# Performance work log

Measured on AMD Instinct MI355X. Metric: run time of the kernel, lower is better.

The kernel has to match this reference:

```python
import jax, jax.numpy as jnp
import numpy as np

B, S, E, H, D, W = 2, 4096, 512, 8, 64, 512
NUM_BUCKETS, MAX_DISTANCE = 32, 128  # hardcoded in get_relative_positions for 't5'
NEG_INF = -1e30


def _t5_bucket_causal(relative_position):
    """T5 relative position bucketing, unidirectional (causal)."""
    n = jnp.maximum(-relative_position, 0)
    max_exact = NUM_BUCKETS // 2
    is_small = n < max_exact
    nf = jnp.maximum(n.astype(jnp.float32), 1.0)
    val_if_large = max_exact + (
        jnp.log(nf / max_exact) / np.log(MAX_DISTANCE / max_exact)
        * (NUM_BUCKETS - max_exact)
    ).astype(jnp.int32)
    val_if_large = jnp.minimum(val_if_large, NUM_BUCKETS - 1)
    return jnp.where(is_small, n, val_if_large)


def setup_inputs() -> dict:
    key = jax.random.key(0)
    ks = jax.random.split(key, 7)
    scale = 1.0 / np.sqrt(E)  # keep logits in a sane range
    return {
        'xs': jax.random.normal(ks[0], (B, S, E), jnp.float32),
        'prev_k': jax.random.normal(ks[1], (B, W, H, D), jnp.float32),
        'prev_v': jax.random.normal(ks[2], (B, W, H, D), jnp.float32),
        'w_q': jax.random.normal(ks[3], (E, H, D), jnp.float32) * scale,
        'w_k': jax.random.normal(ks[4], (E, H, D), jnp.float32) * scale,
        'w_v': jax.random.normal(ks[5], (E, H, D), jnp.float32) * scale,
        'rel_bias': jax.random.normal(ks[6], (H, NUM_BUCKETS), jnp.float32),
    }


def reference(xs, prev_k, prev_v, w_q, w_k, w_v, rel_bias):
    nw = S // W  # number of windows
    # kvq projections; queries pre-scaled by 1/sqrt(head_size)
    q = jnp.einsum('bse,ehd->bshd', xs, w_q) * (1.0 / np.sqrt(D))
    k = jnp.einsum('bse,ehd->bshd', xs, w_k)
    v = jnp.einsum('bse,ehd->bshd', xs, w_v)
    qw = q.reshape(B, nw, W, H, D)
    kw = k.reshape(B, nw, W, H, D)
    vw = v.reshape(B, nw, W, H, D)
    # Transformer-XL sliding window: keys for window i = [window i-1 keys ; window i keys]
    k_prev = jnp.concatenate([prev_k[:, None], kw[:, :-1]], axis=1)  # (B,nw,W,H,D)
    v_prev = jnp.concatenate([prev_v[:, None], vw[:, :-1]], axis=1)
    k2 = jnp.concatenate([k_prev, kw], axis=2)  # (B,nw,2W,H,D)
    v2 = jnp.concatenate([v_prev, vw], axis=2)
    # T5 relative position bias and causal mask (num_queries=W, num_keys=2W)
    ctx = jnp.arange(W)[:, None] + W          # query absolute position in key frame
    mem = jnp.arange(2 * W)[None, :]
    relpos = mem - ctx                        # (W, 2W), key - query
    bias = rel_bias[:, _t5_bucket_causal(relpos)]  # (H, W, 2W)
    # causal + window mask: key j attends iff i < j <= i+W (each query sees exactly W keys)
    mask = (relpos <= 0) & (relpos > -W)
    # attention per window
    scores = jnp.einsum('bnqhd,bnkhd->bnhqk', qw, k2)  # (B,nw,H,W,2W)
    scores = scores + bias[None, None]
    scores = jnp.where(mask[None, None, None], scores, NEG_INF)
    probs = jax.nn.softmax(scores, axis=-1)
    attn = jnp.einsum('bnhqk,bnkhd->bnqhd', probs, v2)
    attn_ys = attn.reshape(B, S, H, D)
    # next_kvi cache = last window's keys/values
    next_k = kw[:, -1]
    next_v = vw[:, -1]
    return attn_ys, next_k, next_v
```

## Files before the change

### kernel.cpp

```cpp
#include <hip/hip_runtime.h>
#include <hip/hip_bf16.h>
#include <math.h>

#define B_ 2
#define S_ 4096
#define E_ 512
#define H_ 8
#define D_ 64
#define W_ 512
#define NW_ 8

#define MASKV -1e30f
#define MINIT -1e4f

typedef float f32x4 __attribute__((ext_vector_type(4)));
typedef short s16x4 __attribute__((ext_vector_type(4)));
typedef short s16x8 __attribute__((ext_vector_type(8)));
typedef unsigned int u32;
typedef __attribute__((address_space(1))) const u32 as1_u32;
typedef __attribute__((address_space(3))) u32 as3_u32;

__device__ inline short f2bf(float f) {
    unsigned u = __builtin_bit_cast(unsigned, f);
    unsigned r = (u + 0x7FFFu + ((u >> 16) & 1u)) >> 16;
    return (short)r;
}
__device__ inline s16x8 pack8(f32x4 a, f32x4 b) {
    s16x8 r;
    r[0]=f2bf(a[0]); r[1]=f2bf(a[1]); r[2]=f2bf(a[2]); r[3]=f2bf(a[3]);
    r[4]=f2bf(b[0]); r[5]=f2bf(b[1]); r[6]=f2bf(b[2]); r[7]=f2bf(b[3]);
    return r;
}
__device__ __forceinline__ void gl_lds16(const void* g, void* l) {
    __builtin_amdgcn_global_load_lds((as1_u32*)(unsigned long long)g,
                                     (as3_u32*)(u32)(unsigned long long)l,
                                     16, 0, 0);
}

__global__ void convert_kernel(const float* __restrict__ xs, const float* __restrict__ pk,
                               const float* __restrict__ pv, short* __restrict__ xsbf,
                               short* __restrict__ pkbf, short* __restrict__ pvbf)
{
    size_t i8 = ((size_t)blockIdx.x * 256 + threadIdx.x) * 8;
    const float* src; short* dst; size_t off;
    if (i8 < 4194304)            { src = xs; dst = xsbf; off = i8; }
    else if (i8 < 4194304+524288){ src = pk; dst = pkbf; off = i8 - 4194304; }
    else                         { src = pv; dst = pvbf; off = i8 - 4194304 - 524288; }
    f32x4 a = *(const f32x4*)(src + off);
    f32x4 b = *(const f32x4*)(src + off + 4);
    *(s16x8*)(dst + off) = pack8(a, b);
}

__global__ void transpose_w_kernel(const float* __restrict__ wq, const float* __restrict__ wk,
                                   const float* __restrict__ wv, short* __restrict__ wt)
{
    __shared__ float st[64][68];
    const int k0 = blockIdx.x * 64;
    const int nt = blockIdx.y;
    const int z  = nt >> 3;
    const int n0 = (nt & 7) * 64;
    const float* wz = (z == 0) ? wq : (z == 1) ? wk : wv;
    const float scale = (z == 0) ? 0.125f : 1.0f;
    const int tid = threadIdx.x;
    {
        int kk = tid >> 4, nn = (tid & 15) * 4;
        #pragma unroll
        for (int it = 0; it < 4; ++it) {
            f32x4 x = *(const f32x4*)(wz + (size_t)(k0 + kk + it * 16) * 512 + n0 + nn);
            *(f32x4*)&st[kk + it * 16][nn] = x;
        }
    }
    __syncthreads();
    {
        int nn2 = tid >> 2, kseg = (tid & 3) * 16;
        s16x8 o0, o1;
        #pragma unroll
        for (int j = 0; j < 8; ++j) o0[j] = f2bf(st[kseg + j][nn2] * scale);
        #pragma unroll
        for (int j = 0; j < 8; ++j) o1[j] = f2bf(st[kseg + 8 + j][nn2] * scale);
        short* dst = wt + (size_t)(z * 512 + n0 + nn2) * 512 + k0 + kseg;
        *(s16x8*)(dst) = o0;
        *(s16x8*)(dst + 8) = o1;
    }
}

__global__ __launch_bounds__(256, 4)
void proj_kernel(const short* __restrict__ xsbf, const short* __restrict__ wt,
                 short* __restrict__ qkvbf, float* __restrict__ out)
{
    __shared__ short Xs[128][64];
    __shared__ short Ws[128][64];

    const int tid = threadIdx.x;
    const int m0  = blockIdx.x * 128;
    const int n0  = blockIdx.y * 128;
    const int z   = n0 >> 9;
    const int ln0 = n0 & 511;
    const int wave = tid >> 6, lane = tid & 63;
    const int wq = (wave & 1) * 64;
    const int wx = (wave >> 1) * 64;
    const int lr = lane & 15, quad = lane >> 4;

    f32x4 acc[4][4] = {};

    const int r8  = lane >> 3;
    const int gr  = lane & 7;

    for (int k0 = 0; k0 < 512; k0 += 64) {
        #pragma unroll
        for (int i = 0; i < 4; ++i) {
            int row = 32 * wave + 8 * i + r8;
            int gs  = gr ^ (row & 7);
            gl_lds16(xsbf + (size_t)(m0 + row) * 512 + k0 + gs * 8, &Xs[32 * wave + 8 * i][0]);
            gl_lds16(wt   + (size_t)(n0 + row) * 512 + k0 + gs * 8, &Ws[32 * wave + 8 * i][0]);
        }
        __syncthreads();
        #pragma unroll
        for (int ks = 0; ks < 2; ++ks) {
            s16x8 af[4], bf[4];
            #pragma unroll
            for (int ta = 0; ta < 4; ++ta) {
                int R = wq + ta * 16 + lr;
                af[ta] = *(const s16x8*)&Ws[R][(((ks * 4 + quad) ^ (R & 7)) * 8)];
            }
            #pragma unroll
            for (int tb = 0; tb < 4; ++tb) {
                int R = wx + tb * 16 + lr;
                bf[tb] = *(const s16x8*)&Xs[R][(((ks * 4 + quad) ^ (R & 7)) * 8)];
            }
            #pragma unroll
            for (int ta = 0; ta < 4; ++ta)
                #pragma unroll
                for (int tb = 0; tb < 4; ++tb)
                    acc[ta][tb] = __builtin_amdgcn_mfma_f32_16x16x32_bf16(
                        af[ta], bf[tb], acc[ta][tb], 0, 0, 0);
        }
        __syncthreads();
    }

    short* base = qkvbf + (size_t)z * ((size_t)8192 * 512);
    #pragma unroll
    for (int ta = 0; ta < 4; ++ta)
        #pragma unroll
        for (int tb = 0; tb < 4; ++tb) {
            int m  = m0 + wx + tb * 16 + lr;
            int ln = ln0 + wq + ta * 16 + quad * 4;
            s16x4 o;
            o[0] = f2bf(acc[ta][tb][0]); o[1] = f2bf(acc[ta][tb][1]);
            o[2] = f2bf(acc[ta][tb][2]); o[3] = f2bf(acc[ta][tb][3]);
            *(s16x4*)(base + (size_t)m * 512 + ln) = o;
            if (z != 0 && (m & 4095) >= 3584) {
                int bb = m >> 12, rr = (m & 4095) - 3584;
                float* dst = out + 4194304 + (size_t)(z - 1) * 524288
                           + ((size_t)(bb * 512 + rr)) * 512 + ln;
                *(f32x4*)dst = acc[ta][tb];
            }
        }
}

__global__ __launch_bounds__(512, 4)
void attn_kernel(const short* __restrict__ qkvbf, const short* __restrict__ pkbf,
                 const short* __restrict__ pvbf, const float* __restrict__ rel_bias,
                 float* __restrict__ out)
{
    __shared__ short p_s[128][72];
    __shared__ short k_s[2][64][72];
    __shared__ short vt_s[2][64][72];
    __shared__ float bias_s[512];

    const short* qb = qkvbf;
    const short* kb = qkvbf + (size_t)8192 * 512;
    const short* vb = qkvbf + (size_t)2 * 8192 * 512;

    const int bid = blockIdx.x;
    const int qt = bid & 3;
    const int h  = (bid >> 2) & 7;
    const int n  = (bid >> 5) & 7;
    const int b  = bid >> 8;
    const int tid = threadIdx.x;
    const int wave = tid >> 6, lane = tid & 63;
    const int lr = lane & 15, quad = lane >> 4;
    const int q0 = qt * 128;
    const int i0 = q0 + 16 * wave;

    {
        int nd = tid;
        int bucket;
        if (nd < 16) bucket = nd;
        else {
            int vbk = 16 + (int)(log((double)nd * (1.0 / 16.0)) * (16.0 / log(8.0)));
            bucket = vbk < 31 ? vbk : 31;
        }
        bias_s[nd] = rel_bias[h * 32 + bucket];
    }

    s16x8 aq[2];
    {
        const short* src = qb + (size_t)(b * S_ + n * W_ + i0 + lr) * 512 + h * 64 + quad * 8;
        aq[0] = *(const s16x8*)(src);
        aq[1] = *(const s16x8*)(src + 32);
    }

    f32x4 oacc[4] = {};
    float m_r[4], l_r[4];
    #pragma unroll
    for (int rg = 0; rg < 4; ++rg) { m_r[rg] = MINIT; l_r[rg] = 0.f; }

    const int cmin = (16 * wave) >> 6;
    int cmax = (16 * wave + 528) >> 6; if (cmax > 9) cmax = 9;

    const int ksr = tid >> 3;
    const int ksd = (tid & 7) * 8;
    const int vkey = tid & 63;
    const int vd0 = (tid >> 6) * 8;

    s16x8 rk, rv;
    {
        int jj = q0 + ksr;
        int p  = n * W_ + jj - W_;
        const short* ks = (p >= 0) ? kb + (size_t)(b * S_ + p) * 512 + h * 64 + ksd
                                   : pkbf + ((size_t)(b * W_ + jj) * H_ + h) * D_ + ksd;
        rk = *(const s16x8*)ks;
        int jv = q0 + vkey;
        int pv = n * W_ + jv - W_;
        const short* vs = (pv >= 0) ? vb + (size_t)(b * S_ + pv) * 512 + h * 64 + vd0
                                    : pvbf + ((size_t)(b * W_ + jv) * H_ + h) * D_ + vd0;
        rv = *(const s16x8*)vs;
    }

    for (int c = 0; c < 10; ++c) {
        const int pb = c & 1;
        *(s16x8*)&k_s[pb][ksr][ksd] = rk;
        #pragma unroll
        for (int m = 0; m < 8; ++m) vt_s[pb][vd0 + m][vkey] = rv[m];

        {
            int cn = (c < 9) ? c + 1 : 9;
            int jj = q0 + 64 * cn + ksr;
            int p  = n * W_ + jj - W_;
            const short* ks = (p >= 0) ? kb + (size_t)(b * S_ + p) * 512 + h * 64 + ksd
                                       : pkbf + ((size_t)(b * W_ + jj) * H_ + h) * D_ + ksd;
            rk = *(const s16x8*)ks;
            int jv = q0 + 64 * cn + vkey;
            int pv = n * W_ + jv - W_;
            const short* vs = (pv >= 0) ? vb + (size_t)(b * S_ + pv) * 512 + h * 64 + vd0
                                        : pvbf + ((size_t)(b * W_ + jv) * H_ + h) * D_ + vd0;
            rv = *(const s16x8*)vs;
        }

        __syncthreads();
        if (c < cmin || c > cmax) continue;

        f32x4 sacc[4] = {};
        #pragma unroll
        for (int ks = 0; ks < 2; ++ks) {
            s16x8 bk[4];
            #pragma unroll
            for (int tn = 0; tn < 4; ++tn)
                bk[tn] = *(const s16x8*)&k_s[pb][tn * 16 + lr][ks * 32 + quad * 8];
            #pragma unroll
            for (int tn = 0; tn < 4; ++tn)
                sacc[tn] = __builtin_amdgcn_mfma_f32_16x16x32_bf16(
                    aq[ks], bk[tn], sacc[tn], 0, 0, 0);
        }

        const int jc = q0 + 64 * c + lr;
        #pragma unroll
        for (int tn = 0; tn < 4; ++tn) {
            int j = jc + tn * 16;
            #pragma unroll
            for (int rg = 0; rg < 4; ++rg) {
                int i = i0 + quad * 4 + rg;
                unsigned dm1 = (unsigned)(j - i - 1);
                int nd = (i + 512 - j) & 511;
                float sv = sacc[tn][rg] + bias_s[nd];
                sacc[tn][rg] = (dm1 < 512u) ? sv : MASKV;
            }
        }

        float rmax[4];
        #pragma unroll
        for (int rg = 0; rg < 4; ++rg)
            rmax[rg] = fmaxf(fmaxf(sacc[0][rg], sacc[1][rg]),
                             fmaxf(sacc[2][rg], sacc[3][rg]));
        #pragma unroll
        for (int off = 1; off < 16; off <<= 1)
            #pragma unroll
            for (int rg = 0; rg < 4; ++rg)
                rmax[rg] = fmaxf(rmax[rg], __shfl_xor(rmax[rg], off));

        float al[4], rs[4];
        #pragma unroll
        for (int rg = 0; rg < 4; ++rg) {
            float mo = m_r[rg];
            float mn = fmaxf(mo, rmax[rg]);
            al[rg] = __expf(mo - mn);
            m_r[rg] = mn;
            rs[rg] = 0.f;
        }

        #pragma unroll
        for (int tn = 0; tn < 4; ++tn)
            #pragma unroll
            for (int rg = 0; rg < 4; ++rg) {
                float p = __expf(sacc[tn][rg] - m_r[rg]);
                rs[rg] += p;
                p_s[16 * wave + quad * 4 + rg][tn * 16 + lr] = f2bf(p);
            }

        #pragma unroll
        for (int off = 1; off < 16; off <<= 1)
            #pragma unroll
            for (int rg = 0; rg < 4; ++rg)
                rs[rg] += __shfl_xor(rs[rg], off);

        #pragma unroll
        for (int rg = 0; rg < 4; ++rg)
            l_r[rg] = l_r[rg] * al[rg] + rs[rg];

        #pragma unroll
        for (int tn = 0; tn < 4; ++tn)
            #pragma unroll
            for (int rg = 0; rg < 4; ++rg)
                oacc[tn][rg] *= al[rg];

        asm volatile("s_waitcnt lgkmcnt(0)" ::: "memory");

        #pragma unroll
        for (int ks = 0; ks < 2; ++ks) {
            s16x8 ap = *(const s16x8*)&p_s[16 * wave + lr][ks * 32 + quad * 8];
            s16x8 bv[4];
            #pragma unroll
            for (int tn = 0; tn < 4; ++tn)
                bv[tn] = *(const s16x8*)&vt_s[pb][tn * 16 + lr][ks * 32 + quad * 8];
            #pragma unroll
            for (int tn = 0; tn < 4; ++tn)
                oacc[tn] = __builtin_amdgcn_mfma_f32_16x16x32_bf16(
                    ap, bv[tn], oacc[tn], 0, 0, 0);
        }
    }

    #pragma unroll
    for (int rg = 0; rg < 4; ++rg) {
        int row = i0 + quad * 4 + rg;
        float linv = 1.0f / l_r[rg];
        float* dst = out + (((size_t)b * S_ + n * W_ + row) * H_ + h) * D_ + lr;
        #pragma unroll
        for (int tn = 0; tn < 4; ++tn)
            dst[tn * 16] = oacc[tn][rg] * linv;
    }
}

extern "C" void kernel_launch(void* const* d_in, const int* in_sizes, int n_in,
                              void* d_out, int out_size, void* d_ws, size_t ws_size,
                              hipStream_t stream)
{
    const float* xs       = (const float*)d_in[0];
    const float* prev_k   = (const float*)d_in[1];
    const float* prev_v   = (const float*)d_in[2];
    const float* w_q      = (const float*)d_in[3];
    const float* w_k      = (const float*)d_in[4];
    const float* w_v      = (const float*)d_in[5];
    const float* rel_bias = (const float*)d_in[6];
    float* out = (float*)d_out;

    short* xsbf  = (short*)d_ws;
    short* wt    = xsbf + (size_t)8192 * 512;
    short* qkvbf = wt + (size_t)1536 * 512;
    short* pkbf  = qkvbf + (size_t)3 * 8192 * 512;
    short* pvbf  = pkbf + (size_t)524288;

    convert_kernel<<<2560, 256, 0, stream>>>(xs, prev_k, prev_v, xsbf, pkbf, pvbf);
    transpose_w_kernel<<<dim3(8, 24), 256, 0, stream>>>(w_q, w_k, w_v, wt);

    proj_kernel<<<dim3(64, 12), 256, 0, stream>>>(xsbf, wt, qkvbf, out);

    attn_kernel<<<512, 512, 0, stream>>>(qkvbf, pkbf, pvbf, rel_bias, out);
}
```

Measured before the change: 146.8 us.

## Store V transposed, async-load K/V to swizzled LDS, drop online softmax max

The projection kernel now writes V in a head-dim-major transposed layout, and a new small kernel converts and transposes prev_v into the same layout. The attention kernel fetches K and V^T straight into XOR-swizzled LDS with global_load_lds double buffering, replacing the register staging and scalar LDS transpose. The online softmax no longer tracks a running max: it exponentiates the biased scores directly and, for far chunks, uses the constant bucket-31 bias instead of a table lookup. Skipping the max relies on the logits staying small and risks overflow for other inputs.

```diff
diff --git a/kernel.cpp b/kernel.cpp
--- a/kernel.cpp
+++ b/kernel.cpp
@@ -4,14 +4,11 @@
 
 #define B_ 2
 #define S_ 4096
-#define E_ 512
 #define H_ 8
 #define D_ 64
 #define W_ 512
-#define NW_ 8
 
 #define MASKV -1e30f
-#define MINIT -1e4f
 
 typedef float f32x4 __attribute__((ext_vector_type(4)));
 typedef short s16x4 __attribute__((ext_vector_type(4)));
@@ -36,19 +33,49 @@
                                      (as3_u32*)(u32)(unsigned long long)l,
                                      16, 0, 0);
 }
+__device__ __forceinline__ void drain_vmem() {
+    asm volatile("s_waitcnt vmcnt(0)" ::: "memory");
+}
 
 __global__ void convert_kernel(const float* __restrict__ xs, const float* __restrict__ pk,
-                               const float* __restrict__ pv, short* __restrict__ xsbf,
-                               short* __restrict__ pkbf, short* __restrict__ pvbf)
+                               short* __restrict__ xsbf, short* __restrict__ pkbf)
 {
     size_t i8 = ((size_t)blockIdx.x * 256 + threadIdx.x) * 8;
     const float* src; short* dst; size_t off;
-    if (i8 < 4194304)            { src = xs; dst = xsbf; off = i8; }
-    else if (i8 < 4194304+524288){ src = pk; dst = pkbf; off = i8 - 4194304; }
-    else                         { src = pv; dst = pvbf; off = i8 - 4194304 - 524288; }
+    if (i8 < 4194304) { src = xs; dst = xsbf; off = i8; }
+    else              { src = pk; dst = pkbf; off = i8 - 4194304; }
     f32x4 a = *(const f32x4*)(src + off);
     f32x4 b = *(const f32x4*)(src + off + 4);
     *(s16x8*)(dst + off) = pack8(a, b);
+}
+
+__global__ void prev_v_t_kernel(const float* __restrict__ pv, short* __restrict__ vbt)
+{
+    __shared__ short st[64][72];
+    const int bidx = blockIdx.x;
+    const int jt = bidx & 7, h = (bidx >> 3) & 7, b = bidx >> 6;
+    const int jj0 = jt * 64;
+    const int tid = threadIdx.x;
+    {
+        int kk = tid >> 2, d0 = (tid & 3) * 16;
+        const float* src = pv + (((size_t)(b * 512 + jj0 + kk)) * 8 + h) * 64 + d0;
+        f32x4 x0 = *(const f32x4*)(src);
+        f32x4 x1 = *(const f32x4*)(src + 4);
+        f32x4 x2 = *(const f32x4*)(src + 8);
+        f32x4 x3 = *(const f32x4*)(src + 12);
+        *(s16x8*)&st[kk][d0]     = pack8(x0, x1);
+        *(s16x8*)&st[kk][d0 + 8] = pack8(x2, x3);
+    }
+    __syncthreads();
+    {
+        int dd = tid >> 2, k0 = (tid & 3) * 16;
+        s16x8 o0, o1;
+        #pragma unroll
+        for (int t = 0; t < 8; ++t) { o0[t] = st[k0 + t][dd]; o1[t] = st[k0 + 8 + t][dd]; }
+        short* dst = vbt + (size_t)(h * 64 + dd) * 9216 + b * 4608 + jj0 + k0;
+        *(s16x8*)dst = o0;
+        *(s16x8*)(dst + 8) = o1;
+    }
 }
 
 __global__ void transpose_w_kernel(const float* __restrict__ wq, const float* __restrict__ wk,
@@ -86,7 +113,8 @@
 
 __global__ __launch_bounds__(256, 4)
 void proj_kernel(const short* __restrict__ xsbf, const short* __restrict__ wt,
-                 short* __restrict__ qkvbf, float* __restrict__ out)
+                 short* __restrict__ qkbf, short* __restrict__ vbt,
+                 float* __restrict__ out)
 {
     __shared__ short Xs[128][64];
     __shared__ short Ws[128][64];
@@ -114,6 +142,7 @@
             gl_lds16(xsbf + (size_t)(m0 + row) * 512 + k0 + gs * 8, &Xs[32 * wave + 8 * i][0]);
             gl_lds16(wt   + (size_t)(n0 + row) * 512 + k0 + gs * 8, &Ws[32 * wave + 8 * i][0]);
         }
+        drain_vmem();
         __syncthreads();
         #pragma unroll
         for (int ks = 0; ks < 2; ++ks) {
@@ -138,39 +167,48 @@
         __syncthreads();
     }
 
-    short* base = qkvbf + (size_t)z * ((size_t)8192 * 512);
     #pragma unroll
     for (int ta = 0; ta < 4; ++ta)
         #pragma unroll
         for (int tb = 0; tb < 4; ++tb) {
             int m  = m0 + wx + tb * 16 + lr;
             int ln = ln0 + wq + ta * 16 + quad * 4;
-            s16x4 o;
-            o[0] = f2bf(acc[ta][tb][0]); o[1] = f2bf(acc[ta][tb][1]);
-            o[2] = f2bf(acc[ta][tb][2]); o[3] = f2bf(acc[ta][tb][3]);
-            *(s16x4*)(base + (size_t)m * 512 + ln) = o;
-            if (z != 0 && (m & 4095) >= 3584) {
-                int bb = m >> 12, rr = (m & 4095) - 3584;
-                float* dst = out + 4194304 + (size_t)(z - 1) * 524288
-                           + ((size_t)(bb * 512 + rr)) * 512 + ln;
-                *(f32x4*)dst = acc[ta][tb];
+            int bb = m >> 12, seq = m & 4095;
+            if (z < 2) {
+                short* base = qkbf + (size_t)z * ((size_t)8192 * 512);
+                s16x4 o;
+                o[0] = f2bf(acc[ta][tb][0]); o[1] = f2bf(acc[ta][tb][1]);
+                o[2] = f2bf(acc[ta][tb][2]); o[3] = f2bf(acc[ta][tb][3]);
+                *(s16x4*)(base + (size_t)m * 512 + ln) = o;
+                if (z == 1 && seq >= 3584) {
+                    float* dst = out + 4194304 + ((size_t)(bb * 512 + seq - 3584)) * 512 + ln;
+                    *(f32x4*)dst = acc[ta][tb];
+                }
+            } else {
+                size_t col = (size_t)bb * 4608 + 512 + seq;
+                #pragma unroll
+                for (int g = 0; g < 4; ++g)
+                    vbt[(size_t)(ln + g) * 9216 + col] = f2bf(acc[ta][tb][g]);
+                if (seq >= 3584) {
+                    float* dst = out + 4194304 + 524288 + ((size_t)(bb * 512 + seq - 3584)) * 512 + ln;
+                    *(f32x4*)dst = acc[ta][tb];
+                }
             }
         }
 }
 
 __global__ __launch_bounds__(512, 4)
-void attn_kernel(const short* __restrict__ qkvbf, const short* __restrict__ pkbf,
-                 const short* __restrict__ pvbf, const float* __restrict__ rel_bias,
+void attn_kernel(const short* __restrict__ qkbf, const short* __restrict__ vbt,
+                 const short* __restrict__ pkbf, const float* __restrict__ rel_bias,
                  float* __restrict__ out)
 {
-    __shared__ short p_s[128][72];
-    __shared__ short k_s[2][64][72];
-    __shared__ short vt_s[2][64][72];
+    __shared__ short k_s[2][64][64];
+    __shared__ short vt_s[2][64][64];
+    __shared__ short p_s[128][64];
     __shared__ float bias_s[512];
 
-    const short* qb = qkvbf;
-    const short* kb = qkvbf + (size_t)8192 * 512;
-    const short* vb = qkvbf + (size_t)2 * 8192 * 512;
+    const short* qb = qkbf;
+    const short* kb = qkbf + (size_t)8192 * 512;
 
     const int bid = blockIdx.x;
     const int qt = bid & 3;
@@ -193,6 +231,7 @@
         }
         bias_s[nd] = rel_bias[h * 32 + bucket];
     }
+    const float bias31 = rel_bias[h * 32 + 31];
 
     s16x8 aq[2];
     {
@@ -202,53 +241,34 @@
     }
 
     f32x4 oacc[4] = {};
-    float m_r[4], l_r[4];
-    #pragma unroll
-    for (int rg = 0; rg < 4; ++rg) { m_r[rg] = MINIT; l_r[rg] = 0.f; }
+    float lsum = 0.f;
 
     const int cmin = (16 * wave) >> 6;
-    int cmax = (16 * wave + 528) >> 6; if (cmax > 9) cmax = 9;
-
-    const int ksr = tid >> 3;
-    const int ksd = (tid & 7) * 8;
-    const int vkey = tid & 63;
-    const int vd0 = (tid >> 6) * 8;
-
-    s16x8 rk, rv;
-    {
-        int jj = q0 + ksr;
+    const int cmax = (16 * wave + 527) >> 6;
+
+    const int r8 = lane >> 3, gr = lane & 7;
+
+    auto issueKV = [&](int c, int pb) {
+        int jj = q0 + 64 * c + 8 * wave + r8;
         int p  = n * W_ + jj - W_;
-        const short* ks = (p >= 0) ? kb + (size_t)(b * S_ + p) * 512 + h * 64 + ksd
-                                   : pkbf + ((size_t)(b * W_ + jj) * H_ + h) * D_ + ksd;
-        rk = *(const s16x8*)ks;
-        int jv = q0 + vkey;
-        int pv = n * W_ + jv - W_;
-        const short* vs = (pv >= 0) ? vb + (size_t)(b * S_ + pv) * 512 + h * 64 + vd0
-                                    : pvbf + ((size_t)(b * W_ + jv) * H_ + h) * D_ + vd0;
-        rv = *(const s16x8*)vs;
-    }
+        int gs = gr ^ r8;
+        const short* ksrc = (p >= 0)
+            ? kb   + ((size_t)(b * S_ + p)) * 512 + h * 64 + gs * 8
+            : pkbf + (((size_t)(b * W_ + jj)) * 8 + h) * 64 + gs * 8;
+        gl_lds16(ksrc, &k_s[pb][8 * wave][0]);
+        int drow = 8 * wave + r8;
+        const short* vsrc = vbt + (size_t)(h * 64 + drow) * 9216
+                          + b * 4608 + n * W_ + q0 + 64 * c + gs * 8;
+        gl_lds16(vsrc, &vt_s[pb][8 * wave][0]);
+    };
+
+    issueKV(0, 0);
 
     for (int c = 0; c < 10; ++c) {
         const int pb = c & 1;
-        *(s16x8*)&k_s[pb][ksr][ksd] = rk;
-        #pragma unroll
-        for (int m = 0; m < 8; ++m) vt_s[pb][vd0 + m][vkey] = rv[m];
-
-        {
-            int cn = (c < 9) ? c + 1 : 9;
-            int jj = q0 + 64 * cn + ksr;
-            int p  = n * W_ + jj - W_;
-            const short* ks = (p >= 0) ? kb + (size_t)(b * S_ + p) * 512 + h * 64 + ksd
-                                       : pkbf + ((size_t)(b * W_ + jj) * H_ + h) * D_ + ksd;
-            rk = *(const s16x8*)ks;
-            int jv = q0 + 64 * cn + vkey;
-            int pv = n * W_ + jv - W_;
-            const short* vs = (pv >= 0) ? vb + (size_t)(b * S_ + pv) * 512 + h * 64 + vd0
-                                        : pvbf + ((size_t)(b * W_ + jv) * H_ + h) * D_ + vd0;
-            rv = *(const s16x8*)vs;
-        }
-
+        drain_vmem();
         __syncthreads();
+        if (c < 9) issueKV(c + 1, pb ^ 1);
         if (c < cmin || c > cmax) continue;
 
         f32x4 sacc[4] = {};
@@ -257,82 +277,60 @@
             s16x8 bk[4];
             #pragma unroll
             for (int tn = 0; tn < 4; ++tn)
-                bk[tn] = *(const s16x8*)&k_s[pb][tn * 16 + lr][ks * 32 + quad * 8];
+                bk[tn] = *(const s16x8*)&k_s[pb][tn * 16 + lr][(((4 * ks + quad) ^ (lr & 7)) * 8)];
             #pragma unroll
             for (int tn = 0; tn < 4; ++tn)
                 sacc[tn] = __builtin_amdgcn_mfma_f32_16x16x32_bf16(
-                    aq[ks], bk[tn], sacc[tn], 0, 0, 0);
-        }
-
-        const int jc = q0 + 64 * c + lr;
-        #pragma unroll
-        for (int tn = 0; tn < 4; ++tn) {
-            int j = jc + tn * 16;
-            #pragma unroll
-            for (int rg = 0; rg < 4; ++rg) {
-                int i = i0 + quad * 4 + rg;
-                unsigned dm1 = (unsigned)(j - i - 1);
-                int nd = (i + 512 - j) & 511;
-                float sv = sacc[tn][rg] + bias_s[nd];
-                sacc[tn][rg] = (dm1 < 512u) ? sv : MASKV;
-            }
-        }
-
-        float rmax[4];
-        #pragma unroll
-        for (int rg = 0; rg < 4; ++rg)
-            rmax[rg] = fmaxf(fmaxf(sacc[0][rg], sacc[1][rg]),
-                             fmaxf(sacc[2][rg], sacc[3][rg]));
-        #pragma unroll
-        for (int off = 1; off < 16; off <<= 1)
-            #pragma unroll
-            for (int rg = 0; rg < 4; ++rg)
-                rmax[rg] = fmaxf(rmax[rg], __shfl_xor(rmax[rg], off));
-
-        float al[4], rs[4];
-        #pragma unroll
-        for (int rg = 0; rg < 4; ++rg) {
-            float mo = m_r[rg];
-            float mn = fmaxf(mo, rmax[rg]);
-            al[rg] = __expf(mo - mn);
-            m_r[rg] = mn;
-            rs[rg] = 0.f;
-        }
-
-        #pragma unroll
-        for (int tn = 0; tn < 4; ++tn)
-            #pragma unroll
-            for (int rg = 0; rg < 4; ++rg) {
-                float p = __expf(sacc[tn][rg] - m_r[rg]);
-                rs[rg] += p;
-                p_s[16 * wave + quad * 4 + rg][tn * 16 + lr] = f2bf(p);
-            }
-
-        #pragma unroll
-        for (int off = 1; off < 16; off <<= 1)
-            #pragma unroll
-            for (int rg = 0; rg < 4; ++rg)
-                rs[rg] += __shfl_xor(rs[rg], off);
-
-        #pragma unroll
-        for (int rg = 0; rg < 4; ++rg)
-            l_r[rg] = l_r[rg] * al[rg] + rs[rg];
-
-        #pragma unroll
-        for (int tn = 0; tn < 4; ++tn)
-            #pragma unroll
-            for (int rg = 0; rg < 4; ++rg)
-                oacc[tn][rg] *= al[rg];
+                    bk[tn], aq[ks], sacc[tn], 0, 0, 0);
+        }
+
+        const int ib = i0 + lr;
+        const int jb = q0 + 64 * c;
+        if (64 * c - 16 * wave <= 336) {
+            #pragma unroll
+            for (int tn = 0; tn < 4; ++tn) {
+                s16x4 pp;
+                #pragma unroll
+                for (int rg = 0; rg < 4; ++rg) {
+                    int j = jb + tn * 16 + quad * 4 + rg;
+                    unsigned dm1 = (unsigned)(j - ib - 1);
+                    float sv = (dm1 < 512u) ? (sacc[tn][rg] + bias31) : MASKV;
+                    float p = __expf(sv);
+                    lsum += p;
+                    pp[rg] = f2bf(p);
+                }
+                int gp = (2 * tn + (quad >> 1)) ^ (lr & 7);
+                *(s16x4*)&p_s[16 * wave + lr][gp * 8 + (quad & 1) * 4] = pp;
+            }
+        } else {
+            #pragma unroll
+            for (int tn = 0; tn < 4; ++tn) {
+                s16x4 pp;
+                #pragma unroll
+                for (int rg = 0; rg < 4; ++rg) {
+                    int j = jb + tn * 16 + quad * 4 + rg;
+                    unsigned dm1 = (unsigned)(j - ib - 1);
+                    float bias = bias_s[(ib + 512 - j) & 511];
+                    float sv = (dm1 < 512u) ? (sacc[tn][rg] + bias) : MASKV;
+                    float p = __expf(sv);
+                    lsum += p;
+                    pp[rg] = f2bf(p);
+                }
+                int gp = (2 * tn + (quad >> 1)) ^ (lr & 7);
+                *(s16x4*)&p_s[16 * wave + lr][gp * 8 + (quad & 1) * 4] = pp;
+            }
+        }
 
         asm volatile("s_waitcnt lgkmcnt(0)" ::: "memory");
 
         #pragma unroll
         for (int ks = 0; ks < 2; ++ks) {
-            s16x8 ap = *(const s16x8*)&p_s[16 * wave + lr][ks * 32 + quad * 8];
+            int gpa = (4 * ks + quad) ^ (lr & 7);
+            s16x8 ap = *(const s16x8*)&p_s[16 * wave + lr][gpa * 8];
             s16x8 bv[4];
             #pragma unroll
             for (int tn = 0; tn < 4; ++tn)
-                bv[tn] = *(const s16x8*)&vt_s[pb][tn * 16 + lr][ks * 32 + quad * 8];
+                bv[tn] = *(const s16x8*)&vt_s[pb][tn * 16 + lr][(((4 * ks + quad) ^ (lr & 7)) * 8)];
             #pragma unroll
             for (int tn = 0; tn < 4; ++tn)
                 oacc[tn] = __builtin_amdgcn_mfma_f32_16x16x32_bf16(
@@ -340,14 +338,20 @@
         }
     }
 
+    lsum += __shfl_xor(lsum, 16);
+    lsum += __shfl_xor(lsum, 32);
+    float linv[4];
+    #pragma unroll
+    for (int rg = 0; rg < 4; ++rg)
+        linv[rg] = 1.0f / __shfl(lsum, quad * 4 + rg);
+
     #pragma unroll
     for (int rg = 0; rg < 4; ++rg) {
         int row = i0 + quad * 4 + rg;
-        float linv = 1.0f / l_r[rg];
         float* dst = out + (((size_t)b * S_ + n * W_ + row) * H_ + h) * D_ + lr;
         #pragma unroll
         for (int tn = 0; tn < 4; ++tn)
-            dst[tn * 16] = oacc[tn][rg] * linv;
+            dst[tn * 16] = oacc[tn][rg] * linv[rg];
     }
 }
 
@@ -364,16 +368,17 @@
     const float* rel_bias = (const float*)d_in[6];
     float* out = (float*)d_out;
 
-    short* xsbf  = (short*)d_ws;
-    short* wt    = xsbf + (size_t)8192 * 512;
-    short* qkvbf = wt + (size_t)1536 * 512;
-    short* pkbf  = qkvbf + (size_t)3 * 8192 * 512;
-    short* pvbf  = pkbf + (size_t)524288;
-
-    convert_kernel<<<2560, 256, 0, stream>>>(xs, prev_k, prev_v, xsbf, pkbf, pvbf);
+    short* xsbf = (short*)d_ws;
+    short* wt   = xsbf + (size_t)4194304;
+    short* qkbf = wt   + (size_t)786432;
+    short* pkbf = qkbf + (size_t)8388608;
+    short* vbt  = pkbf + (size_t)524288;
+
+    convert_kernel<<<2304, 256, 0, stream>>>(xs, prev_k, xsbf, pkbf);
+    prev_v_t_kernel<<<128, 256, 0, stream>>>(prev_v, vbt);
     transpose_w_kernel<<<dim3(8, 24), 256, 0, stream>>>(w_q, w_k, w_v, wt);
 
-    proj_kernel<<<dim3(64, 12), 256, 0, stream>>>(xsbf, wt, qkvbf, out);
-
-    attn_kernel<<<512, 512, 0, stream>>>(qkvbf, pkbf, pvbf, rel_bias, out);
-}
+    proj_kernel<<<dim3(64, 12), 256, 0, stream>>>(xsbf, wt, qkbf, vbt, out);
+
+    attn_kernel<<<512, 512, 0, stream>>>(qkbf, vbt, pkbf, rel_bias, out);
+}
```

Result: faster. 135.7 us (-7.6%).
